# Kernel optimization log

Measured on AMD Instinct MI355X. Metric: run time of the kernel, lower is better.

The kernel has to match this reference:

```python
import jax, jax.numpy as jnp
import numpy as np


def setup_inputs() -> dict:
    key = jax.random.key(0)
    k1, k2 = jax.random.split(key)
    B, HW, C = 256, 196, 384
    x = jax.random.normal(k1, (B, HW + 1, C), dtype=jnp.float32)
    edge_aggregation = jax.random.normal(k2, (B, HW, C), dtype=jnp.float32)
    return {"x": x, "edge_aggregation": edge_aggregation}


def reference(x, edge_aggregation):
    # x: (B, HW+1, C); edge_aggregation: (B, HW, C)
    nodes = x[:, 1:]                                    # (B, HW, C)
    # AvgPool1d over full HW length == mean over token axis
    ea = jnp.mean(edge_aggregation, axis=1, keepdims=True)   # (B, 1, C)
    channel_importance = jax.nn.sigmoid(ea)                  # (B, 1, C)
    # nodes @ channel_importance^T -> (B, HW, 1); keep as (B, HW)
    channel_aggregation = jnp.einsum('bnc,bc->bn', nodes, channel_importance[:, 0])
    # ascending sort indices per sample (matches torch.sort default)
    idx = jnp.argsort(channel_aggregation, axis=1)           # (B, HW)
    nodes_sorted = jnp.take_along_axis(nodes, idx[:, :, None], axis=1)  # (B, HW, C)
    HW = nodes.shape[1]
    start = HW // 4 * 3                                       # keep top quartile
    nodes_pooled = nodes_sorted[:, start:]                    # (B, HW - start, C)
    out = jnp.concatenate([x[:, :1], nodes_pooled], axis=1)   # (B, HW-start+1, C)
    return out
```

## Files before the change

### kernel.cpp

```cpp
#include <hip/hip_runtime.h>
#include <math.h>

#define NB      256
#define NNODES  196
#define NC      384
#define SEQ     197
#define START   147
#define KEEP    49
#define OUTROWS 50

#define NT      960
#define NWAVE   15
#define RG      10
#define C4      96
#define P1IT    20
#define NPW     14

__global__ __launch_bounds__(NT)
void pooling_block_kernel(const float* __restrict__ x,
                          const float* __restrict__ ea,
                          float* __restrict__ out) {
    __shared__ double partial[RG][NC];
    __shared__ alignas(16) float imp[NC];
    __shared__ float scores[NNODES];
    __shared__ int   sel[KEEP];

    const int b   = blockIdx.x;
    const int tid = threadIdx.x;

    {
        const int rg = tid / C4;
        const int c4 = tid % C4;
        const float4* p = (const float4*)(ea + (size_t)b * NNODES * NC) + c4;
        float4 v[P1IT];
        #pragma unroll
        for (int it = 0; it < P1IT; ++it) {
            int row = rg + RG * it;
            int r   = row < NNODES ? row : NNODES - 1;
            v[it] = p[(size_t)r * C4];
        }
        double ax = 0.0, ay = 0.0, az = 0.0, aw = 0.0;
        #pragma unroll
        for (int it = 0; it < P1IT; ++it) {
            int row = rg + RG * it;
            float pred = row < NNODES ? 1.0f : 0.0f;
            ax += (double)(pred * v[it].x);
            ay += (double)(pred * v[it].y);
            az += (double)(pred * v[it].z);
            aw += (double)(pred * v[it].w);
        }
        partial[rg][4 * c4 + 0] = ax;
        partial[rg][4 * c4 + 1] = ay;
        partial[rg][4 * c4 + 2] = az;
        partial[rg][4 * c4 + 3] = aw;
    }
    __syncthreads();
    if (tid < NC) {
        double s = 0.0;
        #pragma unroll
        for (int rg = 0; rg < RG; ++rg) s += partial[rg][tid];
        float m = (float)(s * (1.0 / (double)NNODES));
        imp[tid] = 1.0f / (1.0f + expf(-m));
    }
    __syncthreads();

    {
        const int wave = tid >> 6;
        const int lane = tid & 63;
        const int wbase = wave * NPW;
        const float* nodes = x + ((size_t)b * SEQ + 1) * NC;
        const float2* imp2 = (const float2*)imp;

        float2 w[3];
        #pragma unroll
        for (int j = 0; j < 3; ++j) w[j] = imp2[lane + 64 * j];

        #pragma unroll
        for (int c = 0; c < 2; ++c) {
            float2 vv[7][3];
            #pragma unroll
            for (int i = 0; i < 7; ++i) {
                int n  = wbase + c * 7 + i;
                int nn = n < NNODES ? n : NNODES - 1;
                const float2* row2 = (const float2*)(nodes + (size_t)nn * NC);
                #pragma unroll
                for (int j = 0; j < 3; ++j) vv[i][j] = row2[lane + 64 * j];
            }
            #pragma unroll
            for (int i = 0; i < 7; ++i) {
                double acc = 0.0;
                #pragma unroll
                for (int j = 0; j < 3; ++j)
                    acc += (double)vv[i][j].x * (double)w[j].x
                         + (double)vv[i][j].y * (double)w[j].y;
                #pragma unroll
                for (int off = 32; off > 0; off >>= 1)
                    acc += __shfl_xor(acc, off);
                int n = wbase + c * 7 + i;
                if (lane == 0 && n < NNODES) scores[n] = (float)acc;
            }
        }
    }
    __syncthreads();

    if (tid < NNODES) {
        const float s = scores[tid];
        int rank = 0;
        for (int m = 0; m < NNODES; ++m) {
            const float sm = scores[m];
            rank += (sm < s) || (sm == s && m < tid);
        }
        if (rank >= START) sel[rank - START] = tid;
    }
    __syncthreads();

    {
        const int jg = tid / C4;
        const int c4 = tid % C4;
        const float* nodes = x + ((size_t)b * SEQ + 1) * NC;
        const float4* nodes4 = (const float4*)nodes;
        const float4* cls4   = (const float4*)(x + (size_t)b * SEQ * NC);
        float4* out4         = (float4*)(out + (size_t)b * OUTROWS * NC);
        #pragma unroll
        for (int it = 0; it < 5; ++it) {
            int j = jg + RG * it;
            const float4* src = (j == 0) ? cls4 : (nodes4 + (size_t)sel[j - 1] * C4);
            out4[(size_t)j * C4 + c4] = src[c4];
        }
    }
}

extern "C" void kernel_launch(void* const* d_in, const int* in_sizes, int n_in,
                              void* d_out, int out_size, void* d_ws, size_t ws_size,
                              hipStream_t stream) {
    const float* x   = (const float*)d_in[0];
    const float* ea  = (const float*)d_in[1];
    float* out       = (float*)d_out;

    hipLaunchKernelGGL(pooling_block_kernel,
                       dim3(NB), dim3(NT), 0, stream,
                       x, ea, out);
}
```

Baseline: 37.70 us.

## Prefetch first half of node rows before the channel-mean phase

Issues the global loads for each wave's first seven node rows at kernel start, so they are in flight while the edge_aggregation mean and sigmoid are computed. This overlaps the x-read latency with phase one instead of leaving the two phases serialized. The phase-one mean loop also changes from a fully unrolled 20-load batch to a plain strided loop, which lowers register pressure to make room for the 42 prefetched float2 values but gives less memory-level parallelism in that phase. Register pressure at 960 threads per block could cause spills.

```diff
diff --git a/kernel.cpp b/kernel.cpp
--- a/kernel.cpp
+++ b/kernel.cpp
@@ -13,7 +13,6 @@
 #define NWAVE   15
 #define RG      10
 #define C4      96
-#define P1IT    20
 #define NPW     14
 
 __global__ __launch_bounds__(NT)
@@ -25,29 +24,31 @@
     __shared__ float scores[NNODES];
     __shared__ int   sel[KEEP];
 
-    const int b   = blockIdx.x;
-    const int tid = threadIdx.x;
+    const int b    = blockIdx.x;
+    const int tid  = threadIdx.x;
+    const int wave = tid >> 6;
+    const int lane = tid & 63;
+    const int wbase = wave * NPW;
+    const float* nodes = x + ((size_t)b * SEQ + 1) * NC;
+
+    float2 vv0[7][3];
+    #pragma unroll
+    for (int i = 0; i < 7; ++i) {
+        int n  = wbase + i;
+        int nn = n < NNODES ? n : NNODES - 1;
+        const float2* row2 = (const float2*)(nodes + (size_t)nn * NC);
+        #pragma unroll
+        for (int j = 0; j < 3; ++j) vv0[i][j] = row2[lane + 64 * j];
+    }
 
     {
         const int rg = tid / C4;
         const int c4 = tid % C4;
-        const float4* p = (const float4*)(ea + (size_t)b * NNODES * NC) + c4;
-        float4 v[P1IT];
-        #pragma unroll
-        for (int it = 0; it < P1IT; ++it) {
-            int row = rg + RG * it;
-            int r   = row < NNODES ? row : NNODES - 1;
-            v[it] = p[(size_t)r * C4];
-        }
+        const float4* p = (const float4*)(ea + (size_t)b * NNODES * NC);
         double ax = 0.0, ay = 0.0, az = 0.0, aw = 0.0;
-        #pragma unroll
-        for (int it = 0; it < P1IT; ++it) {
-            int row = rg + RG * it;
-            float pred = row < NNODES ? 1.0f : 0.0f;
-            ax += (double)(pred * v[it].x);
-            ay += (double)(pred * v[it].y);
-            az += (double)(pred * v[it].z);
-            aw += (double)(pred * v[it].w);
+        for (int row = rg; row < NNODES; row += RG) {
+            float4 v = p[(size_t)row * C4 + c4];
+            ax += v.x; ay += v.y; az += v.z; aw += v.w;
         }
         partial[rg][4 * c4 + 0] = ax;
         partial[rg][4 * c4 + 1] = ay;
@@ -64,41 +65,47 @@
     }
     __syncthreads();
 
+    const float2* imp2 = (const float2*)imp;
+    float2 w[3];
+    #pragma unroll
+    for (int j = 0; j < 3; ++j) w[j] = imp2[lane + 64 * j];
+
+    #pragma unroll
+    for (int i = 0; i < 7; ++i) {
+        double acc = 0.0;
+        #pragma unroll
+        for (int j = 0; j < 3; ++j)
+            acc += (double)vv0[i][j].x * (double)w[j].x
+                 + (double)vv0[i][j].y * (double)w[j].y;
+        #pragma unroll
+        for (int off = 32; off > 0; off >>= 1)
+            acc += __shfl_xor(acc, off);
+        int n = wbase + i;
+        if (lane == 0 && n < NNODES) scores[n] = (float)acc;
+    }
+
     {
-        const int wave = tid >> 6;
-        const int lane = tid & 63;
-        const int wbase = wave * NPW;
-        const float* nodes = x + ((size_t)b * SEQ + 1) * NC;
-        const float2* imp2 = (const float2*)imp;
-
-        float2 w[3];
+        float2 vv1[7][3];
         #pragma unroll
-        for (int j = 0; j < 3; ++j) w[j] = imp2[lane + 64 * j];
-
+        for (int i = 0; i < 7; ++i) {
+            int n  = wbase + 7 + i;
+            int nn = n < NNODES ? n : NNODES - 1;
+            const float2* row2 = (const float2*)(nodes + (size_t)nn * NC);
+            #pragma unroll
+            for (int j = 0; j < 3; ++j) vv1[i][j] = row2[lane + 64 * j];
+        }
         #pragma unroll
-        for (int c = 0; c < 2; ++c) {
-            float2 vv[7][3];
+        for (int i = 0; i < 7; ++i) {
+            double acc = 0.0;
             #pragma unroll
-            for (int i = 0; i < 7; ++i) {
-                int n  = wbase + c * 7 + i;
-                int nn = n < NNODES ? n : NNODES - 1;
-                const float2* row2 = (const float2*)(nodes + (size_t)nn * NC);
-                #pragma unroll
-                for (int j = 0; j < 3; ++j) vv[i][j] = row2[lane + 64 * j];
-            }
+            for (int j = 0; j < 3; ++j)
+                acc += (double)vv1[i][j].x * (double)w[j].x
+                     + (double)vv1[i][j].y * (double)w[j].y;
             #pragma unroll
-            for (int i = 0; i < 7; ++i) {
-                double acc = 0.0;
-                #pragma unroll
-                for (int j = 0; j < 3; ++j)
-                    acc += (double)vv[i][j].x * (double)w[j].x
-                         + (double)vv[i][j].y * (double)w[j].y;
-                #pragma unroll
-                for (int off = 32; off > 0; off >>= 1)
-                    acc += __shfl_xor(acc, off);
-                int n = wbase + c * 7 + i;
-                if (lane == 0 && n < NNODES) scores[n] = (float)acc;
-            }
+            for (int off = 32; off > 0; off >>= 1)
+                acc += __shfl_xor(acc, off);
+            int n = wbase + 7 + i;
+            if (lane == 0 && n < NNODES) scores[n] = (float)acc;
         }
     }
     __syncthreads();
@@ -117,13 +124,12 @@
     {
         const int jg = tid / C4;
         const int c4 = tid % C4;
-        const float* nodes = x + ((size_t)b * SEQ + 1) * NC;
         const float4* nodes4 = (const float4*)nodes;
         const float4* cls4   = (const float4*)(x + (size_t)b * SEQ * NC);
         float4* out4         = (float4*)(out + (size_t)b * OUTROWS * NC);
         #pragma unroll
         for (int it = 0; it < 5; ++it) {
-            int j = jg + RG * it;
+            int j = jg + 10 * it;
             const float4* src = (j == 0) ? cls4 : (nodes4 + (size_t)sel[j - 1] * C4);
             out4[(size_t)j * C4 + c4] = src[c4];
         }
```

Result: slower. 39.60 us (+5.1%).
